# Kernel tuning notes

Measured on AMD Instinct MI355X. Metric: run time of the kernel, lower is better.

The kernel has to match this reference:

```python
import jax, jax.numpy as jnp
import numpy as np

B, D, H, G, E = 32768, 256, 256, 8, 8  # batch, input_size, hidden_size, num_groups, experts_per_group


def setup_inputs() -> dict:
    key = jax.random.key(0)
    ks = jax.random.split(key, 5)
    s_d = 1.0 / np.sqrt(D)
    return {
        "x": jax.random.normal(ks[0], (B, D), dtype=jnp.float32),
        # gate: nn.Linear(D, G*E)
        "W_gate": jax.random.uniform(ks[1], (G * E, D), jnp.float32, -s_d, s_d),
        "b_gate": jax.random.uniform(ks[2], (G * E,), jnp.float32, -s_d, s_d),
        # experts: [G, E] x nn.Linear(D, H)
        "W_exp": jax.random.uniform(ks[3], (G, E, H, D), jnp.float32, -s_d, s_d),
        "b_exp": jax.random.uniform(ks[4], (G, E, H), jnp.float32, -s_d, s_d),
    }


def reference(x, W_gate, b_gate, W_exp, b_exp):
    # gate_outputs = softmax(gate(x), dim=1)  -> [B, G*E]
    gate = jax.nn.softmax(x @ W_gate.T + b_gate, axis=1)
    # per-group sum over experts of Linear(x): contract input dim i and expert dim e
    # [B, G, H]
    group_out = jnp.einsum("bi,gehi->bgh", x, W_exp) + b_exp.sum(axis=1)
    expert_flat = group_out.reshape(x.shape[0], -1)  # [B, G*H]
    # output = sum_g gate[b,g] * expert_flat[b,h]  == gate.sum(1) * expert_flat
    # (avoids materializing the [B, G*E, G*H] broadcast the torch code creates)
    out = gate.sum(axis=1, keepdims=True) * expert_flat
    return out
```

## Files before the change

kernel.cpp:

```cpp
#include <hip/hip_runtime.h>


typedef unsigned short u16;
typedef __bf16 bf16x8 __attribute__((ext_vector_type(8)));
typedef float f32x4 __attribute__((ext_vector_type(4)));

#define MB 32768
#define NN 2048
#define KK 256
#define BK 64

__device__ __forceinline__ u16 f2bf(float f) {
    unsigned u = __builtin_bit_cast(unsigned, f);
    u += 0x7FFFu + ((u >> 16) & 1u);
    return (u16)(u >> 16);
}

__device__ __forceinline__ unsigned cvtpk(float lo, float hi) {
    unsigned r;
    asm("v_cvt_pk_bf16_f32 %0, %1, %2" : "=v"(r) : "v"(lo), "v"(hi));
    return r;
}

__device__ __forceinline__ void gld16(const void* g, void* l) {
    __builtin_amdgcn_global_load_lds((const __attribute__((address_space(1))) void*)g,
                                     (__attribute__((address_space(3))) void*)l,
                                     16, 0, 0);
}

__global__ __launch_bounds__(256) void prep_kernel(
    const float* __restrict__ Wexp, const float* __restrict__ bexp,
    u16* __restrict__ Ws, float* __restrict__ bs)
{
    const int tid = blockIdx.x * 256 + threadIdx.x;
    const int n = tid >> 6;
    const int i = (tid & 63) << 2;
    const int g = n >> 8, h = n & 255;
    const float* base = Wexp + ((size_t)(g * 8) * 256 + h) * 256 + i;
    float s0 = 0.f, s1 = 0.f, s2 = 0.f, s3 = 0.f;
#pragma unroll
    for (int e = 0; e < 8; ++e) {
        const float4 v = *(const float4*)(base + (size_t)e * 65536);
        s0 += v.x; s1 += v.y; s2 += v.z; s3 += v.w;
    }
    ushort4 o;
    o.x = f2bf(s0); o.y = f2bf(s1); o.z = f2bf(s2); o.w = f2bf(s3);
    *(ushort4*)(Ws + (size_t)n * KK + i) = o;
    if ((tid & 63) == 0) {
        float sb = 0.f;
#pragma unroll
        for (int e = 0; e < 8; ++e) sb += bexp[(g * 8 + e) * 256 + h];
        bs[n] = sb;
    }
}

__global__ __launch_bounds__(256, 3) void gemm_kernel(
    const float* __restrict__ X, const u16* __restrict__ Bt,
    const float* __restrict__ bias, float* __restrict__ C)
{
    __shared__ __align__(16) u16 sA[128 * BK];
    __shared__ __align__(16) u16 sB[128 * BK];

    const int t = threadIdx.x;

    const int bid  = blockIdx.x;
    const int rmap = (bid & 7) * 512 + (bid >> 3);
    const int n0 = (rmap & 15) << 7;
    const int m0 = (rmap >> 4) << 7;

    const int lane = t & 63;
    const int w = t >> 6;
    const int wm = (w & 1) << 6;
    const int wn = (w >> 1) << 6;
    const int lr = lane & 15;
    const int quad = lane >> 4;

    f32x4 acc[4][4] = {};

    const int srow = t >> 3;
    const int scs  = t & 7;

    for (int k0 = 0; k0 < KK; k0 += BK) {
#pragma unroll
        for (int r = 0; r < 4; ++r) {
            const int row = srow + r * 32;
            const int gc  = ((scs ^ (row & 7)) << 3);
            gld16(Bt + (size_t)(n0 + row) * KK + k0 + gc, sB + (size_t)(r * 256 + t) * 8);
        }
        f32x4 va[8];
#pragma unroll
        for (int r = 0; r < 4; ++r) {
            const float* src = X + (size_t)(m0 + srow + r * 32) * KK + k0 + (scs << 3);
            va[2 * r]     = *(const f32x4*)(src);
            va[2 * r + 1] = *(const f32x4*)(src + 4);
        }
#pragma unroll
        for (int r = 0; r < 4; ++r) {
            const int row = srow + r * 32;
            const int sc  = (scs ^ (row & 7)) << 3;
            uint4 pk;
            pk.x = cvtpk(va[2 * r][0], va[2 * r][1]);
            pk.y = cvtpk(va[2 * r][2], va[2 * r][3]);
            pk.z = cvtpk(va[2 * r + 1][0], va[2 * r + 1][1]);
            pk.w = cvtpk(va[2 * r + 1][2], va[2 * r + 1][3]);
            *(uint4*)(sA + row * BK + sc) = pk;
        }
        __syncthreads();

#pragma unroll
        for (int kk = 0; kk < 2; ++kk) {
            bf16x8 af[4], bf[4];
#pragma unroll
            for (int mi = 0; mi < 4; ++mi) {
                const int rr = wm + mi * 16 + lr;
                const int c  = (kk * 4 + quad) ^ (rr & 7);
                af[mi] = *(const bf16x8*)(sA + rr * BK + (c << 3));
            }
#pragma unroll
            for (int ni = 0; ni < 4; ++ni) {
                const int rr = wn + ni * 16 + lr;
                const int c  = (kk * 4 + quad) ^ (rr & 7);
                bf[ni] = *(const bf16x8*)(sB + rr * BK + (c << 3));
            }
#pragma unroll
            for (int mi = 0; mi < 4; ++mi)
#pragma unroll
                for (int ni = 0; ni < 4; ++ni)
                    acc[mi][ni] = __builtin_amdgcn_mfma_f32_16x16x32_bf16(
                        af[mi], bf[ni], acc[mi][ni], 0, 0, 0);
        }
        __syncthreads();
    }

#pragma unroll
    for (int ni = 0; ni < 4; ++ni) {
        const int col = n0 + wn + ni * 16 + lr;
        const float bv = bias[col];
#pragma unroll
        for (int mi = 0; mi < 4; ++mi) {
            const int row = m0 + wm + mi * 16 + quad * 4;
            float* Cp = C + (size_t)row * NN + col;
#pragma unroll
            for (int r = 0; r < 4; ++r)
                Cp[(size_t)r * NN] = acc[mi][ni][r] + bv;
        }
    }
}

extern "C" void kernel_launch(void* const* d_in, const int* in_sizes, int n_in,
                              void* d_out, int out_size, void* d_ws, size_t ws_size,
                              hipStream_t stream) {
    const float* x    = (const float*)d_in[0];
    const float* Wexp = (const float*)d_in[3];
    const float* bexp = (const float*)d_in[4];
    float* out = (float*)d_out;

    u16*   Ws = (u16*)d_ws;
    float* bs = (float*)((char*)d_ws + 1048576);

    prep_kernel<<<512, 256, 0, stream>>>(Wexp, bexp, Ws, bs);
    dim3 grid(4096);
    gemm_kernel<<<grid, 256, 0, stream>>>(x, Ws, bs, out);
}
```

Before: 378.3 us.

## Stage fp32 X tiles directly into LDS and convert to bf16 at fragment load

X tiles now go straight from global memory into LDS as fp32 with direct global-to-LDS loads and an XOR swizzle, instead of passing through registers for bf16 packing. The bf16 conversion moves to the point where each wave reads its A fragments, so every block repeats it on its own. The aim is to cut register pressure and the VALU/LDS-write cost on the load path. In exchange LDS use doubles (32KB A tile), which can limit occupancy, and the custom block-index remap is replaced by a plain 2D grid, giving up the L2 locality that remap provided.

```diff
diff --git a/kernel.cpp b/kernel.cpp
--- a/kernel.cpp
+++ b/kernel.cpp
@@ -58,15 +58,12 @@
     const float* __restrict__ X, const u16* __restrict__ Bt,
     const float* __restrict__ bias, float* __restrict__ C)
 {
-    __shared__ __align__(16) u16 sA[128 * BK];
-    __shared__ __align__(16) u16 sB[128 * BK];
+    __shared__ __align__(16) float sA[128 * BK];
+    __shared__ __align__(16) u16   sB[128 * BK];
 
     const int t = threadIdx.x;
-
-    const int bid  = blockIdx.x;
-    const int rmap = (bid & 7) * 512 + (bid >> 3);
-    const int n0 = (rmap & 15) << 7;
-    const int m0 = (rmap >> 4) << 7;
+    const int n0 = blockIdx.x * 128;
+    const int m0 = blockIdx.y * 128;
 
     const int lane = t & 63;
     const int w = t >> 6;
@@ -77,57 +74,55 @@
 
     f32x4 acc[4][4] = {};
 
-    const int srow = t >> 3;
-    const int scs  = t & 7;
+    const int arow = t >> 4;
+    const int aq   = t & 15;
+    const int brow = t >> 3;
+    const int bcs  = t & 7;
 
     for (int k0 = 0; k0 < KK; k0 += BK) {
 #pragma unroll
         for (int r = 0; r < 4; ++r) {
-            const int row = srow + r * 32;
-            const int gc  = ((scs ^ (row & 7)) << 3);
+            const int row = brow + r * 32;
+            const int gc  = ((bcs ^ (row & 7)) << 3);
             gld16(Bt + (size_t)(n0 + row) * KK + k0 + gc, sB + (size_t)(r * 256 + t) * 8);
         }
-        f32x4 va[8];
 #pragma unroll
-        for (int r = 0; r < 4; ++r) {
-            const float* src = X + (size_t)(m0 + srow + r * 32) * KK + k0 + (scs << 3);
-            va[2 * r]     = *(const f32x4*)(src);
-            va[2 * r + 1] = *(const f32x4*)(src + 4);
-        }
-#pragma unroll
-        for (int r = 0; r < 4; ++r) {
-            const int row = srow + r * 32;
-            const int sc  = (scs ^ (row & 7)) << 3;
-            uint4 pk;
-            pk.x = cvtpk(va[2 * r][0], va[2 * r][1]);
-            pk.y = cvtpk(va[2 * r][2], va[2 * r][3]);
-            pk.z = cvtpk(va[2 * r + 1][0], va[2 * r + 1][1]);
-            pk.w = cvtpk(va[2 * r + 1][2], va[2 * r + 1][3]);
-            *(uint4*)(sA + row * BK + sc) = pk;
+        for (int r = 0; r < 8; ++r) {
+            const int row = arow + r * 16;
+            const int q   = aq ^ (row & 15);
+            gld16(X + (size_t)(m0 + row) * KK + k0 + (q << 2), sA + (size_t)(r * 256 + t) * 4);
         }
         __syncthreads();
 
 #pragma unroll
         for (int kk = 0; kk < 2; ++kk) {
-            bf16x8 af[4], bf[4];
+            bf16x8 af[4], bfr[4];
 #pragma unroll
             for (int mi = 0; mi < 4; ++mi) {
                 const int rr = wm + mi * 16 + lr;
-                const int c  = (kk * 4 + quad) ^ (rr & 7);
-                af[mi] = *(const bf16x8*)(sA + rr * BK + (c << 3));
+                const int m  = rr & 15;
+                const int q0 = kk * 8 + quad * 2;
+                const f32x4 lo = *(const f32x4*)(sA + rr * BK + ((q0 ^ m) << 2));
+                const f32x4 hi = *(const f32x4*)(sA + rr * BK + (((q0 ^ m) ^ 1) << 2));
+                union { bf16x8 v; unsigned u[4]; } tmp;
+                tmp.u[0] = cvtpk(lo[0], lo[1]);
+                tmp.u[1] = cvtpk(lo[2], lo[3]);
+                tmp.u[2] = cvtpk(hi[0], hi[1]);
+                tmp.u[3] = cvtpk(hi[2], hi[3]);
+                af[mi] = tmp.v;
             }
 #pragma unroll
             for (int ni = 0; ni < 4; ++ni) {
                 const int rr = wn + ni * 16 + lr;
                 const int c  = (kk * 4 + quad) ^ (rr & 7);
-                bf[ni] = *(const bf16x8*)(sB + rr * BK + (c << 3));
+                bfr[ni] = *(const bf16x8*)(sB + rr * BK + (c << 3));
             }
 #pragma unroll
             for (int mi = 0; mi < 4; ++mi)
 #pragma unroll
                 for (int ni = 0; ni < 4; ++ni)
                     acc[mi][ni] = __builtin_amdgcn_mfma_f32_16x16x32_bf16(
-                        af[mi], bf[ni], acc[mi][ni], 0, 0, 0);
+                        af[mi], bfr[ni], acc[mi][ni], 0, 0, 0);
         }
         __syncthreads();
     }
@@ -159,6 +154,6 @@
     float* bs = (float*)((char*)d_ws + 1048576);
 
     prep_kernel<<<512, 256, 0, stream>>>(Wexp, bexp, Ws, bs);
-    dim3 grid(4096);
+    dim3 grid(NN / 128, MB / 128);
     gemm_kernel<<<grid, 256, 0, stream>>>(x, Ws, bs, out);
 }
```

Measured after the change: 357.0 us. 5.6% less time.
